# Kernel optimization log

Hardware: AMD Instinct MI355X
Metric: run time of the kernel (lower is better)

The kernel has to match this reference:

```python
import jax, jax.numpy as jnp
import numpy as np

BS, S, D, H = 4, 2048, 1024, 4096
TEMP, THRESH, PRIOR, EPS = 1.0, 0.5, 0.2, 1e-9


def setup_inputs() -> dict:
    key = jax.random.key(0)
    ks = jax.random.split(key, 4)
    hidden = jax.random.normal(ks[0], (BS, S, D), jnp.float32)
    # ragged valid lengths to exercise the padding / forced-last-boundary path
    lengths = jnp.array([S, S - 300, S - 700, S // 2], jnp.int32)
    attention_mask = (jnp.arange(S)[None, :] < lengths[:, None]).astype(jnp.float32)
    noise_u = jax.random.uniform(ks[1], (BS, S), jnp.float32, 1e-6, 1.0 - 1e-6)
    W1 = jax.random.normal(ks[2], (D, H), jnp.float32) * (1.0 / np.sqrt(D))
    b1 = jnp.zeros((H,), jnp.float32)
    W2 = jax.random.normal(ks[3], (H,), jnp.float32) * (1.0 / np.sqrt(H))
    b2 = jnp.zeros((), jnp.float32)
    return dict(hidden=hidden, attention_mask=attention_mask, noise_u=noise_u,
                W1=W1, b1=b1, W2=W2, b2=b2)


def reference(hidden, attention_mask, noise_u, W1, b1, W2, b2):
    bs, seq, _ = hidden.shape
    # tiny MLP gate -> per-token boundary logit
    h = jax.nn.relu(jnp.einsum('bsd,dh->bsh', hidden, W1) + b1)
    logits = jnp.einsum('bsh,h->bs', h, W2) + b2                     # [B,S]
    # RelaxedBernoulli(temp, probs=sigmoid(logits)).rsample()
    logistic = jnp.log(noise_u) - jnp.log1p(-noise_u)
    soft = jax.nn.sigmoid((logits + logistic) / TEMP)
    # straight-through hard boundaries
    hard = (soft > THRESH).astype(soft.dtype)
    hard = jax.lax.stop_gradient(hard - soft) + soft
    # mask out padding, force a boundary on the last real token of each row
    hard = hard * attention_mask
    pad = attention_mask == 0
    first_pad = pad & (jnp.cumsum(pad.astype(jnp.int32), axis=1) == 1)
    last_real = jnp.roll(first_pad, shift=-1, axis=1)
    last_real = last_real.at[:, -1].set(False)
    hard = jnp.maximum(hard, last_real.astype(hard.dtype))
    # downsample: mean-pool tokens within segments ending at boundary tokens
    hh1 = jnp.cumsum(hard, axis=1) - hard                            # [B,S] segment id of each token
    foo = jnp.arange(seq, dtype=hard.dtype)[None, None, :] - hh1[:, :, None]  # [B,S_tok,S_seg]
    lel = jnp.where(foo == 0, 1.0 - foo, 0.0)                        # one-hot (diff. via -foo)
    bar = lel / (jnp.sum(lel, axis=1, keepdims=True) + EPS)          # normalize per segment
    pooled = jnp.einsum('bld,bls->bsd', hidden, bar)                 # [B,S_seg,D] (zero-padded beyond max #segments)
    # binomial boundary-rate loss
    num_b = jnp.sum(hard)
    total = jnp.sum(attention_mask)
    gln = jax.scipy.special.gammaln
    log_prob = (gln(total + 1.0) - gln(num_b + 1.0) - gln(total - num_b + 1.0)
                + num_b * jnp.log(PRIOR) + (total - num_b) * jnp.log(1.0 - PRIOR))
    loss = -log_prob / total
    # shortened attention mask: kept positions all have mask==1, so it is a
    # left-packed ones mask of length = #boundaries per row (zero-padded to S)
    counts = jnp.sum(jax.lax.stop_gradient(hard), axis=1)
    short_mask = (jnp.arange(seq, dtype=counts.dtype)[None, :] < counts[:, None]).astype(jnp.float32)
    return pooled, loss, num_b, total, short_mask
```

## Files before the change

### kernel.cpp

```cpp
#include <hip/hip_runtime.h>
#include <math.h>

#define BSZ 4
#define SEQ 2048
#define DIM 1024
#define HID 4096
#define MTOT (BSZ * SEQ)
#define NHB 64
#define EPSF 1e-9f

#define BM 256
#define BN 256
#define BKF 32
#define KITERS (DIM / BKF)
#define BSCALE 32.0f
#define INV_BSCALE (1.0f / 32.0f)

typedef _Float16 f16;
typedef _Float16 f16x4 __attribute__((ext_vector_type(4)));
typedef _Float16 f16x8 __attribute__((ext_vector_type(8)));
typedef float f32x16 __attribute__((ext_vector_type(16)));

__device__ __forceinline__ void gl16(const f16* g, f16* l) {
  __builtin_amdgcn_global_load_lds(
      (const __attribute__((address_space(1))) void*)g,
      (__attribute__((address_space(3))) void*)l, 16, 0, 0);
}

__global__ void split_a(const float* __restrict__ in, f16* __restrict__ hi,
                        f16* __restrict__ lo) {
  int i = blockIdx.x * 256 + threadIdx.x;
  float4 v = ((const float4*)in)[i];
  f16x4 h, l;
  h.x = (f16)v.x; h.y = (f16)v.y; h.z = (f16)v.z; h.w = (f16)v.w;
  l.x = (f16)(v.x - (float)h.x);
  l.y = (f16)(v.y - (float)h.y);
  l.z = (f16)(v.z - (float)h.z);
  l.w = (f16)(v.w - (float)h.w);
  ((f16x4*)hi)[i] = h;
  ((f16x4*)lo)[i] = l;
}

__global__ void split_w1t(const float* __restrict__ w1, f16* __restrict__ hi,
                          f16* __restrict__ lo) {
  __shared__ float tile[32][36];
  const int k0 = blockIdx.x * 32;
  const int h0 = blockIdx.y * 32;
  const int t = threadIdx.x;
  {
    int kk = t >> 3, hq = (t & 7) * 4;
    float4 v = *(const float4*)&w1[(size_t)(k0 + kk) * HID + h0 + hq];
    tile[kk][hq + 0] = v.x; tile[kk][hq + 1] = v.y;
    tile[kk][hq + 2] = v.z; tile[kk][hq + 3] = v.w;
  }
  __syncthreads();
  int hh = t >> 3, kq = (t & 7) * 4;
  f16x4 H, L;
#pragma unroll
  for (int j = 0; j < 4; ++j) {
    float x = tile[kq + j][hh] * BSCALE;
    f16 xh = (f16)x;
    H[j] = xh;
    L[j] = (f16)(x - (float)xh);
  }
  *(f16x4*)&hi[(size_t)(h0 + hh) * DIM + k0 + kq] = H;
  *(f16x4*)&lo[(size_t)(h0 + hh) * DIM + k0 + kq] = L;
}

__global__ __launch_bounds__(512, 2)
void gate_gemm(const f16* __restrict__ Ahi, const f16* __restrict__ Alo,
               const f16* __restrict__ Whi, const f16* __restrict__ Wlo,
               const float* __restrict__ b1, const float* __restrict__ W2,
               float* __restrict__ partial) {
  __shared__ f16 sA[2][BM][64];
  __shared__ f16 sB[2][BN][64];

  const int bid = blockIdx.x;
  const int wg = (bid & 7) * 64 + (bid >> 3);
  const int nt = wg >> 5;
  const int mt = wg & 31;
  const int m0 = mt * BM, h0 = nt * BN;

  const int t = threadIdx.x;
  const int lane = t & 63, wid = t >> 6;
  const int wm = wid >> 2, wn = wid & 3;
  const int rowl = lane & 31, kb = lane >> 5;

  f32x16 acc[4][2];
#pragma unroll
  for (int a = 0; a < 4; ++a)
#pragma unroll
    for (int b = 0; b < 2; ++b)
#pragma unroll
      for (int e = 0; e < 16; ++e) acc[a][b][e] = 0.f;

  const f16* srcA[4];
  const f16* srcB[4];
#pragma unroll
  for (int i = 0; i < 4; ++i) {
    int sig = i * 512 + t;
    int r = sig >> 3, p = sig & 7;
    int q = p ^ (r & 7);
    int koff = (q & 3) * 8;
    srcA[i] = (q < 4 ? Ahi : Alo) + (size_t)(m0 + r) * DIM + koff;
    srcB[i] = (q < 4 ? Whi : Wlo) + (size_t)(h0 + r) * DIM + koff;
  }

#define STAGE(buf, kt)                                                        \
  {                                                                           \
    _Pragma("unroll") for (int i = 0; i < 4; ++i) {                           \
      int ho = (i * 512 + wid * 64) * 8;                                      \
      gl16(srcA[i] + (size_t)(kt) * BKF, &sA[buf][0][0] + ho);                \
      gl16(srcB[i] + (size_t)(kt) * BKF, &sB[buf][0][0] + ho);                \
    }                                                                         \
  }

  STAGE(0, 0);
  __syncthreads();

  for (int kt = 0; kt < KITERS; ++kt) {
    const int buf = kt & 1;
    if (kt + 1 < KITERS) STAGE(buf ^ 1, kt + 1);
#pragma unroll
    for (int ks = 0; ks < 2; ++ks) {
      f16x8 ah[4], al[4], bh[2], bl[2];
      const int sl = ks * 2 + kb;
#pragma unroll
      for (int fm = 0; fm < 4; ++fm) {
        int ra = wm * 128 + fm * 32 + rowl;
        int ph = (sl ^ (ra & 7)) * 8;
        ah[fm] = *(const f16x8*)&sA[buf][ra][ph];
        al[fm] = *(const f16x8*)&sA[buf][ra][ph ^ 32];
      }
#pragma unroll
      for (int fn = 0; fn < 2; ++fn) {
        int rb = wn * 64 + fn * 32 + rowl;
        int pb = (sl ^ (rb & 7)) * 8;
        bh[fn] = *(const f16x8*)&sB[buf][rb][pb];
        bl[fn] = *(const f16x8*)&sB[buf][rb][pb ^ 32];
      }
#pragma unroll
      for (int fm = 0; fm < 4; ++fm)
#pragma unroll
        for (int fn = 0; fn < 2; ++fn)
          acc[fm][fn] = __builtin_amdgcn_mfma_f32_32x32x16_f16(
              ah[fm], bh[fn], acc[fm][fn], 0, 0, 0);
#pragma unroll
      for (int fm = 0; fm < 4; ++fm)
#pragma unroll
        for (int fn = 0; fn < 2; ++fn)
          acc[fm][fn] = __builtin_amdgcn_mfma_f32_32x32x16_f16(
              ah[fm], bl[fn], acc[fm][fn], 0, 0, 0);
#pragma unroll
      for (int fm = 0; fm < 4; ++fm)
#pragma unroll
        for (int fn = 0; fn < 2; ++fn)
          acc[fm][fn] = __builtin_amdgcn_mfma_f32_32x32x16_f16(
              al[fm], bh[fn], acc[fm][fn], 0, 0, 0);
    }
    __syncthreads();
  }

  float b1v[2], w2v[2];
#pragma unroll
  for (int fn = 0; fn < 2; ++fn) {
    int h = h0 + wn * 64 + fn * 32 + rowl;
    b1v[fn] = b1[h];
    w2v[fn] = W2[h];
  }
#pragma unroll
  for (int fm = 0; fm < 4; ++fm)
#pragma unroll
    for (int r = 0; r < 16; ++r) {
      float v0 = acc[fm][0][r] * INV_BSCALE + b1v[0];
      float v1 = acc[fm][1][r] * INV_BSCALE + b1v[1];
      acc[fm][0][r] = fmaxf(v0, 0.f) * w2v[0] + fmaxf(v1, 0.f) * w2v[1];
    }
#pragma unroll
  for (int off = 1; off <= 16; off <<= 1)
#pragma unroll
    for (int fm = 0; fm < 4; ++fm)
#pragma unroll
      for (int r = 0; r < 16; ++r)
        acc[fm][0][r] += __shfl_xor(acc[fm][0][r], off);
  if (rowl == 0) {
    const int hb = nt * 4 + wn;
#pragma unroll
    for (int fm = 0; fm < 4; ++fm)
#pragma unroll
      for (int r = 0; r < 16; ++r) {
        int token = m0 + wm * 128 + fm * 32 + (r & 3) + 8 * (r >> 2) + 4 * kb;
        partial[(size_t)hb * MTOT + token] = acc[fm][0][r];
      }
  }
}

__global__ void reduce_logits(const float* __restrict__ partial,
                              float* __restrict__ logits) {
  int s = blockIdx.x * 256 + threadIdx.x;
  float lg = 0.f;
#pragma unroll
  for (int h = 0; h < NHB; ++h) lg += partial[(size_t)h * MTOT + s];
  logits[s] = lg;
}

__global__ void boundary_scan(const float* __restrict__ logits,
                              const float* __restrict__ mask,
                              const float* __restrict__ noise,
                              const float* __restrict__ b2,
                              int* __restrict__ bpos, int* __restrict__ counts,
                              int* __restrict__ lengths,
                              float* __restrict__ shortmask) {
  const int b = blockIdx.x;
  const int t = threadIdx.x;
  __shared__ float hardS[SEQ];
  __shared__ float red[256];
  const float bias2 = b2[0];

  float msum = 0.f;
  for (int s = t; s < SEQ; s += 256) {
    float lg = logits[b * SEQ + s] + bias2;
    float u = noise[b * SEQ + s];
    float lgt = logf(u) - log1pf(-u);
    float m = mask[b * SEQ + s];
    float hard = ((lg + lgt) > 0.f) ? 1.f : 0.f;
    hardS[s] = hard * m;
    msum += m;
  }
  red[t] = msum;
  __syncthreads();
  for (int off = 128; off > 0; off >>= 1) {
    if (t < off) red[t] += red[t + off];
    __syncthreads();
  }
  int L = (int)(red[0] + 0.5f);
  __syncthreads();
  if (t == 0) {
    if (L < SEQ) hardS[L - 1] = fmaxf(hardS[L - 1], 1.f);
    lengths[b] = L;
  }
  __syncthreads();

  float loc[8];
  float run = 0.f;
#pragma unroll
  for (int i = 0; i < 8; ++i) { loc[i] = hardS[t * 8 + i]; run += loc[i]; }
  red[t] = run;
  __syncthreads();
  for (int off = 1; off < 256; off <<= 1) {
    float v = (t >= off) ? red[t - off] : 0.f;
    __syncthreads();
    red[t] += v;
    __syncthreads();
  }
  float base = red[t] - run;
  int cnt = (int)(red[255] + 0.5f);

  float pre = base;
#pragma unroll
  for (int i = 0; i < 8; ++i) {
    if (loc[i] > 0.5f) {
      int rank = (int)(pre + 0.5f);
      bpos[b * SEQ + rank] = t * 8 + i;
    }
    pre += loc[i];
  }
  if (t == 0) counts[b] = cnt;
  for (int s = t; s < SEQ; s += 256)
    shortmask[b * SEQ + s] = (s < cnt) ? 1.f : 0.f;
}

__global__ void pool_seg(const float* __restrict__ hidden,
                         const int* __restrict__ bpos,
                         const int* __restrict__ counts,
                         float* __restrict__ pooled) {
  const int g = blockIdx.x, b = blockIdx.y;
  const int t = threadIdx.x;
  const int cnt = counts[b];
  float4 acc = {0.f, 0.f, 0.f, 0.f};
  float* outp = pooled + ((size_t)(b * SEQ + g)) * DIM + t * 4;
  if (g > cnt) { *(float4*)outp = acc; return; }
  if (g == cnt) return;
  int start = (g == 0) ? 0 : bpos[b * SEQ + g - 1] + 1;
  int end = bpos[b * SEQ + g] + 1;
  const float* hb = hidden + ((size_t)b * SEQ) * DIM + t * 4;
  for (int l = start; l < end; ++l) {
    float4 v = *(const float4*)(hb + (size_t)l * DIM);
    acc.x += v.x; acc.y += v.y; acc.z += v.z; acc.w += v.w;
  }
  float inv = 1.f / ((float)(end - start) + EPSF);
  acc.x *= inv; acc.y *= inv; acc.z *= inv; acc.w *= inv;
  *(float4*)outp = acc;
}

__global__ void pool_tail_partial(const float* __restrict__ hidden,
                                  const int* __restrict__ bpos,
                                  const int* __restrict__ counts,
                                  float* __restrict__ tailpart) {
  const int c = blockIdx.x;
  const int b = blockIdx.y;
  const int t = threadIdx.x;
  int cnt = counts[b];
  int start = (cnt == 0) ? 0 : bpos[b * SEQ + cnt - 1] + 1;
  int n = SEQ - start;
  int clen = (n + 15) / 16;
  int s0 = start + c * clen;
  int s1 = s0 + clen; if (s1 > SEQ) s1 = SEQ;
  float4 acc = {0.f, 0.f, 0.f, 0.f};
  const float* hb = hidden + ((size_t)b * SEQ) * DIM + t * 4;
  for (int l = s0; l < s1; ++l) {
    float4 v = *(const float4*)(hb + (size_t)l * DIM);
    acc.x += v.x; acc.y += v.y; acc.z += v.z; acc.w += v.w;
  }
  *(float4*)(tailpart + ((size_t)(b * 16 + c)) * DIM + t * 4) = acc;
}

__global__ void pool_tail_final(const int* __restrict__ bpos,
                                const int* __restrict__ counts,
                                const float* __restrict__ tailpart,
                                float* __restrict__ pooled) {
  const int b = blockIdx.x;
  const int t = threadIdx.x;
  int cnt = counts[b];
  if (cnt >= SEQ) return;
  int start = (cnt == 0) ? 0 : bpos[b * SEQ + cnt - 1] + 1;
  float4 acc = {0.f, 0.f, 0.f, 0.f};
  for (int c = 0; c < 16; ++c) {
    float4 v = *(const float4*)(tailpart + ((size_t)(b * 16 + c)) * DIM + t * 4);
    acc.x += v.x; acc.y += v.y; acc.z += v.z; acc.w += v.w;
  }
  float inv = 1.f / ((float)(SEQ - start) + EPSF);
  acc.x *= inv; acc.y *= inv; acc.z *= inv; acc.w *= inv;
  *(float4*)(pooled + ((size_t)(b * SEQ + cnt)) * DIM + t * 4) = acc;
}

__global__ void loss_kernel(const int* __restrict__ counts,
                            const int* __restrict__ lengths,
                            float* __restrict__ outScalars) {
  if (threadIdx.x != 0 || blockIdx.x != 0) return;
  double num_b = 0.0, total = 0.0;
  for (int b = 0; b < BSZ; ++b) { num_b += (double)counts[b]; total += (double)lengths[b]; }
  double lp = lgamma(total + 1.0) - lgamma(num_b + 1.0) - lgamma(total - num_b + 1.0)
            + num_b * log(0.2) + (total - num_b) * log(0.8);
  outScalars[0] = (float)(-lp / total);
  outScalars[1] = (float)num_b;
  outScalars[2] = (float)total;
}

extern "C" void kernel_launch(void* const* d_in, const int* in_sizes, int n_in,
                              void* d_out, int out_size, void* d_ws, size_t ws_size,
                              hipStream_t stream) {
  const float* hidden = (const float*)d_in[0];
  const float* mask   = (const float*)d_in[1];
  const float* noise  = (const float*)d_in[2];
  const float* W1     = (const float*)d_in[3];
  const float* b1     = (const float*)d_in[4];
  const float* W2     = (const float*)d_in[5];
  const float* b2     = (const float*)d_in[6];

  float* out = (float*)d_out;
  float* pooled = out;
  float* scalars = out + (size_t)BSZ * SEQ * DIM;
  float* shortmask = scalars + 3;

  char* ws = (char*)d_ws;
  size_t off = 0;
  float* partial = (float*)(ws + off); off += (size_t)NHB * MTOT * sizeof(float);
  f16* Ahi = (f16*)(ws + off); off += (size_t)MTOT * DIM * sizeof(f16);
  f16* Alo = (f16*)(ws + off); off += (size_t)MTOT * DIM * sizeof(f16);
  f16* Whi = (f16*)(ws + off); off += (size_t)HID * DIM * sizeof(f16);
  f16* Wlo = (f16*)(ws + off); off += (size_t)HID * DIM * sizeof(f16);
  float* logits = (float*)(ws + off); off += (size_t)MTOT * sizeof(float);
  int* bpos = (int*)(ws + off); off += (size_t)BSZ * SEQ * sizeof(int);
  int* counts = (int*)(ws + off); off += 16 * sizeof(int);
  int* lengths = (int*)(ws + off); off += 16 * sizeof(int);
  off = (off + 255) & ~(size_t)255;
  float* tailpart = (float*)(ws + off);

  split_a<<<MTOT * DIM / 4 / 256, 256, 0, stream>>>(hidden, Ahi, Alo);
  split_w1t<<<dim3(DIM / 32, HID / 32), 256, 0, stream>>>(W1, Whi, Wlo);
  gate_gemm<<<(MTOT / BM) * (HID / BN), 512, 0, stream>>>(Ahi, Alo, Whi, Wlo,
                                                          b1, W2, partial);
  reduce_logits<<<MTOT / 256, 256, 0, stream>>>(partial, logits);
  boundary_scan<<<BSZ, 256, 0, stream>>>(logits, mask, noise, b2,
                                         bpos, counts, lengths, shortmask);
  pool_tail_partial<<<dim3(16, BSZ), 256, 0, stream>>>(hidden, bpos, counts, tailpart);
  pool_seg<<<dim3(SEQ, BSZ), 256, 0, stream>>>(hidden, bpos, counts, pooled);
  pool_tail_final<<<BSZ, 256, 0, stream>>>(bpos, counts, tailpart, pooled);
  loss_kernel<<<1, 1, 0, stream>>>(counts, lengths, scalars);
}
```

Measured before the change: 271.6 us.

## Split GEMM main loop into four phases interleaving staging, LDS reads and MFMA

Restructures the gate GEMM k-loop into four phases. Each phase issues a slice of the next tile's global-to-LDS loads, reads a half-fragment from LDS and runs a 12-MFMA cluster. Explicit s_barrier, sched_barrier, vmcnt/lgkmcnt waits and s_setprio around the MFMA clusters replace the compiler-scheduled loop with a single __syncthreads. The goal is to overlap memory traffic with matrix math and lower register pressure by holding half the A fragments at a time. The cost is more barriers per iteration and fragile hand-placed wait counts that could race if miscounted.

After: 269.5 us. About the same (-0.8%).

```diff
diff --git a/kernel.cpp b/kernel.cpp
--- a/kernel.cpp
+++ b/kernel.cpp
@@ -85,6 +85,7 @@
   const int lane = t & 63, wid = t >> 6;
   const int wm = wid >> 2, wn = wid & 3;
   const int rowl = lane & 31, kb = lane >> 5;
+  const int sl0 = kb, sl1 = 2 + kb;
 
   f32x16 acc[4][2];
 #pragma unroll
@@ -106,59 +107,105 @@
     srcB[i] = (q < 4 ? Whi : Wlo) + (size_t)(h0 + r) * DIM + koff;
   }
 
-#define STAGE(buf, kt)                                                        \
-  {                                                                           \
-    _Pragma("unroll") for (int i = 0; i < 4; ++i) {                           \
-      int ho = (i * 512 + wid * 64) * 8;                                      \
-      gl16(srcA[i] + (size_t)(kt) * BKF, &sA[buf][0][0] + ho);                \
-      gl16(srcB[i] + (size_t)(kt) * BKF, &sB[buf][0][0] + ho);                \
-    }                                                                         \
-  }
-
-  STAGE(0, 0);
-  __syncthreads();
+#define STAGE_B2(buf_, kt_, j)                                                \
+  { _Pragma("unroll") for (int i = 2 * (j); i < 2 * (j) + 2; ++i) {           \
+      gl16(srcB[i] + (size_t)(kt_) * BKF,                                     \
+           &sB[buf_][0][0] + (i * 512 + wid * 64) * 8);                       \
+  } }
+#define STAGE_A2(buf_, kt_, j)                                                \
+  { _Pragma("unroll") for (int ii = 0; ii < 2; ++ii) {                        \
+      int i = (j) + ii * 2;                                                   \
+      gl16(srcA[i] + (size_t)(kt_) * BKF,                                     \
+           &sA[buf_][0][0] + (i * 512 + wid * 64) * 8);                       \
+  } }
+
+#define LDA2(fmb, sl)                                                         \
+  { _Pragma("unroll") for (int f = 0; f < 2; ++f) {                           \
+      int ra = wm * 128 + ((fmb) + f) * 32 + rowl;                            \
+      int ph = ((sl) ^ (ra & 7)) * 8;                                         \
+      ah[f] = *(const f16x8*)&sA[buf][ra][ph];                                \
+      al[f] = *(const f16x8*)&sA[buf][ra][ph ^ 32];                           \
+  } }
+#define LDB2(sl)                                                              \
+  { _Pragma("unroll") for (int n = 0; n < 2; ++n) {                           \
+      int rb = wn * 64 + n * 32 + rowl;                                       \
+      int pb = ((sl) ^ (rb & 7)) * 8;                                         \
+      bh[n] = *(const f16x8*)&sB[buf][rb][pb];                                \
+      bl[n] = *(const f16x8*)&sB[buf][rb][pb ^ 32];                           \
+  } }
+
+#define MFMA12(fmb)                                                           \
+  { _Pragma("unroll") for (int f = 0; f < 2; ++f)                             \
+      _Pragma("unroll") for (int n = 0; n < 2; ++n)                           \
+        acc[(fmb) + f][n] = __builtin_amdgcn_mfma_f32_32x32x16_f16(           \
+            ah[f], bh[n], acc[(fmb) + f][n], 0, 0, 0);                        \
+    _Pragma("unroll") for (int f = 0; f < 2; ++f)                             \
+      _Pragma("unroll") for (int n = 0; n < 2; ++n)                           \
+        acc[(fmb) + f][n] = __builtin_amdgcn_mfma_f32_32x32x16_f16(           \
+            ah[f], bl[n], acc[(fmb) + f][n], 0, 0, 0);                        \
+    _Pragma("unroll") for (int f = 0; f < 2; ++f)                             \
+      _Pragma("unroll") for (int n = 0; n < 2; ++n)                           \
+        acc[(fmb) + f][n] = __builtin_amdgcn_mfma_f32_32x32x16_f16(           \
+            al[f], bh[n], acc[(fmb) + f][n], 0, 0, 0); }
+
+#define SBAR                                                                  \
+  { __builtin_amdgcn_sched_barrier(0); __builtin_amdgcn_s_barrier();          \
+    __builtin_amdgcn_sched_barrier(0); }
+#define LGKM0                                                                 \
+  { asm volatile("s_waitcnt lgkmcnt(0)" ::: "memory");                        \
+    __builtin_amdgcn_sched_barrier(0); }
+
+  STAGE_B2(0, 0, 0); STAGE_B2(0, 0, 1);
+  STAGE_A2(0, 0, 0); STAGE_A2(0, 0, 1);
+  asm volatile("s_waitcnt vmcnt(2)" ::: "memory");
+  SBAR;
 
   for (int kt = 0; kt < KITERS; ++kt) {
     const int buf = kt & 1;
-    if (kt + 1 < KITERS) STAGE(buf ^ 1, kt + 1);
-#pragma unroll
-    for (int ks = 0; ks < 2; ++ks) {
-      f16x8 ah[4], al[4], bh[2], bl[2];
-      const int sl = ks * 2 + kb;
-#pragma unroll
-      for (int fm = 0; fm < 4; ++fm) {
-        int ra = wm * 128 + fm * 32 + rowl;
-        int ph = (sl ^ (ra & 7)) * 8;
-        ah[fm] = *(const f16x8*)&sA[buf][ra][ph];
-        al[fm] = *(const f16x8*)&sA[buf][ra][ph ^ 32];
-      }
-#pragma unroll
-      for (int fn = 0; fn < 2; ++fn) {
-        int rb = wn * 64 + fn * 32 + rowl;
-        int pb = (sl ^ (rb & 7)) * 8;
-        bh[fn] = *(const f16x8*)&sB[buf][rb][pb];
-        bl[fn] = *(const f16x8*)&sB[buf][rb][pb ^ 32];
-      }
-#pragma unroll
-      for (int fm = 0; fm < 4; ++fm)
-#pragma unroll
-        for (int fn = 0; fn < 2; ++fn)
-          acc[fm][fn] = __builtin_amdgcn_mfma_f32_32x32x16_f16(
-              ah[fm], bh[fn], acc[fm][fn], 0, 0, 0);
-#pragma unroll
-      for (int fm = 0; fm < 4; ++fm)
-#pragma unroll
-        for (int fn = 0; fn < 2; ++fn)
-          acc[fm][fn] = __builtin_amdgcn_mfma_f32_32x32x16_f16(
-              ah[fm], bl[fn], acc[fm][fn], 0, 0, 0);
-#pragma unroll
-      for (int fm = 0; fm < 4; ++fm)
-#pragma unroll
-        for (int fn = 0; fn < 2; ++fn)
-          acc[fm][fn] = __builtin_amdgcn_mfma_f32_32x32x16_f16(
-              al[fm], bh[fn], acc[fm][fn], 0, 0, 0);
-    }
-    __syncthreads();
+    const int nbuf = buf ^ 1;
+    const bool notlast = (kt + 1 < KITERS);
+    f16x8 ah[2], al[2], bh[2], bl[2];
+
+    LDA2(0, sl0); LDB2(sl0);
+    if (notlast) STAGE_B2(nbuf, kt + 1, 0);
+    SBAR;
+    LGKM0;
+    __builtin_amdgcn_s_setprio(1);
+    MFMA12(0);
+    __builtin_amdgcn_s_setprio(0);
+    __builtin_amdgcn_sched_barrier(0);
+    if (notlast) { asm volatile("s_waitcnt vmcnt(2)" ::: "memory"); }
+    else         { asm volatile("s_waitcnt vmcnt(0)" ::: "memory"); }
+    SBAR;
+
+    LDA2(2, sl0);
+    if (notlast) STAGE_B2(nbuf, kt + 1, 1);
+    SBAR;
+    LGKM0;
+    __builtin_amdgcn_s_setprio(1);
+    MFMA12(2);
+    __builtin_amdgcn_s_setprio(0);
+    SBAR;
+
+    LDA2(0, sl1); LDB2(sl1);
+    if (notlast) STAGE_A2(nbuf, kt + 1, 0);
+    SBAR;
+    LGKM0;
+    __builtin_amdgcn_s_setprio(1);
+    MFMA12(0);
+    __builtin_amdgcn_s_setprio(0);
+    SBAR;
+
+    LDA2(2, sl1);
+    if (notlast) STAGE_A2(nbuf, kt + 1, 1);
+    SBAR;
+    LGKM0;
+    __builtin_amdgcn_s_setprio(1);
+    MFMA12(2);
+    __builtin_amdgcn_s_setprio(0);
+    __builtin_amdgcn_sched_barrier(0);
+    if (notlast) { asm volatile("s_waitcnt vmcnt(2)" ::: "memory"); }
+    SBAR;
   }
 
   float b1v[2], w2v[2];
```
